# Kernel optimization log

Measured on AMD Instinct MI355X. Metric: run time of the kernel, lower is better.

Reference implementation:

```python
import jax, jax.numpy as jnp
import numpy as np

B, NQ, NC = 256, 15, 30          # pairs, query size, corpus size (= max_set_size)
EQ, EC = 45, 90                  # original directed edges per query / corpus graph
ENEW = NQ * (NC - NQ)            # edges added to pad each query graph
NPG = 2 * NC                     # nodes per pair after padding
N = B * NPG                      # 15360 total nodes
E = B * (EQ + EC + ENEW)         # 92160 total edges
D = 128                          # node_state_dim == filters_3
T = 64                           # transform_dim
N_PROP = 5
SK_ITERS, SK_TEMP = 10, 0.1


def _glorot(rng, shape):
    fan_in, fan_out = shape[0], shape[-1]
    s = np.sqrt(2.0 / (fan_in + fan_out))
    return jnp.asarray(rng.standard_normal(shape) * s, dtype=jnp.float32)


def setup_inputs() -> dict:
    rng = np.random.default_rng(0)
    frs, tos = [], []
    # original edges, grouped per pair as (query graph, corpus graph)
    for i in range(B):
        qoff, coff = i * NPG, i * NPG + NC
        frs.append(rng.integers(0, NQ, EQ) + qoff)
        tos.append(rng.integers(0, NQ, EQ) + qoff)
        frs.append(rng.integers(0, NC, EC) + coff)
        tos.append(rng.integers(0, NC, EC) + coff)
    # new padding edges: from each original query node to each new node
    for i in range(B):
        qoff = i * NPG
        frs.append(np.repeat(np.arange(NQ), NC - NQ) + qoff)
        tos.append(np.tile(np.arange(NQ, NC), NQ) + qoff)
    from_idx = jnp.asarray(np.concatenate(frs), dtype=jnp.int32)
    to_idx = jnp.asarray(np.concatenate(tos), dtype=jnp.int32)
    n_orig = B * (EQ + EC)
    mask_from_idx = jnp.concatenate([jnp.ones(n_orig), jnp.zeros(E - n_orig)]).astype(jnp.float32)
    inp = {
        'node_features': jnp.ones((N, 1), jnp.float32),
        'edge_features': jnp.ones((E, 1), jnp.float32),
        'mask_from_idx': mask_from_idx,
        'enc_node_w': _glorot(rng, (1, D)), 'enc_node_b': jnp.zeros(D, jnp.float32),
        'enc_edge_w': _glorot(rng, (1, D)), 'enc_edge_b': jnp.zeros(D, jnp.float32),
        'msg_w1': _glorot(rng, (3 * D, 2 * D)), 'msg_b1': jnp.zeros(2 * D, jnp.float32),
        'msg_w2': _glorot(rng, (2 * D, D)), 'msg_b2': jnp.zeros(D, jnp.float32),
        'upd_w1': _glorot(rng, (2 * D, 2 * D)), 'upd_b1': jnp.zeros(2 * D, jnp.float32),
        'upd_w2': _glorot(rng, (2 * D, D)), 'upd_b2': jnp.zeros(D, jnp.float32),
        'ft1_w': _glorot(rng, (D, T)), 'ft1_b': jnp.zeros(T, jnp.float32),
        'ft2_w': _glorot(rng, (T, T)), 'ft2_b': jnp.zeros(T, jnp.float32),
        'from_idx': from_idx, 'to_idx': to_idx,
    }
    return inp


def reference(node_features, edge_features, mask_from_idx,
              enc_node_w, enc_node_b, enc_edge_w, enc_edge_b,
              msg_w1, msg_b1, msg_w2, msg_b2,
              upd_w1, upd_b1, upd_w2, upd_b2,
              ft1_w, ft1_b, ft2_w, ft2_b,
              from_idx, to_idx):
    # GraphEncoder: linear embed of all-ones node/edge features
    h = node_features @ enc_node_w + enc_node_b          # [N, D]
    e = edge_features @ enc_edge_w + enc_edge_b          # [E, D]
    m = mask_from_idx[:, None]
    # shared GraphPropLayer applied n_prop_layers times
    for _ in range(N_PROP):
        msg_in = jnp.concatenate([h[from_idx], h[to_idx], e], axis=-1)      # [E, 3D]
        msg = jax.nn.relu(msg_in @ msg_w1 + msg_b1) @ msg_w2 + msg_b2       # [E, D]
        agg = jax.ops.segment_sum(msg * m, to_idx, num_segments=N)          # [N, D]
        upd_in = jnp.concatenate([agg, h], axis=-1)                          # [N, 2D]
        h = h + (jax.nn.relu(upd_in @ upd_w1 + upd_b1) @ upd_w2 + upd_b2)   # residual update
    hp = h.reshape(B, 2, NC, D)
    q_emb, c_emb = hp[:, 0], hp[:, 1]                    # [B, NC, D] each
    def transform(x):
        return jax.nn.relu(x @ ft1_w + ft1_b) @ ft2_w + ft2_b
    # query mask: only first NQ (original) nodes kept; corpus graphs are full size
    q_mask = (jnp.arange(NC) < NQ).astype(h.dtype)[None, :, None]
    tq = transform(q_emb) * q_mask                       # [B, NC, T]
    tc = transform(c_emb)                                # [B, NC, T]
    log_alpha = jnp.einsum('bqt,bct->bqc', tq, tc) / SK_TEMP
    for _ in range(SK_ITERS):
        log_alpha = log_alpha - jax.nn.logsumexp(log_alpha, axis=2, keepdims=True)
        log_alpha = log_alpha - jax.nn.logsumexp(log_alpha, axis=1, keepdims=True)
    tp = jnp.exp(log_alpha)                              # [B, NC, NC] transport plan
    moved = jnp.einsum('bqc,bcd->bqd', tp, c_emb)
    scores = -jnp.sum(jax.nn.relu(q_emb - moved), axis=(1, 2))  # [B]
    return scores
```

## Files before the change

kernel.cpp:

```cpp
#include <hip/hip_runtime.h>

#define BATCH 256
#define D 128
#define TT 64
#define NPG 60
#define NCC 30
#define NQQ 15
#define EPG 135
#define NPROP 5
#define SKI 10

typedef __attribute__((ext_vector_type(8))) short bf16x8;
typedef __attribute__((ext_vector_type(4))) float f32x4;

union U8 { bf16x8 v; uint4 u; };

__device__ __forceinline__ unsigned short f2bf(float f) {
    union { float f; unsigned int i; } t;
    t.f = f;
    unsigned int r = t.i + 0x7fffu + ((t.i >> 16) & 1u);
    return (unsigned short)(r >> 16);
}
__device__ __forceinline__ float bf2f(unsigned short u) {
    union { float f; unsigned int i; } t;
    t.i = ((unsigned int)u) << 16;
    return t.f;
}
__device__ __forceinline__ void split_bf(float v, unsigned short& hi, unsigned short& lo) {
    hi = f2bf(v);
    lo = f2bf(v - bf2f(hi));
}

__device__ __forceinline__ void splitv(float4 a, float4 b, bf16x8& hi, bf16x8& lo) {
    unsigned int ia0=__float_as_uint(a.x), ia1=__float_as_uint(a.y);
    unsigned int ia2=__float_as_uint(a.z), ia3=__float_as_uint(a.w);
    unsigned int ib0=__float_as_uint(b.x), ib1=__float_as_uint(b.y);
    unsigned int ib2=__float_as_uint(b.z), ib3=__float_as_uint(b.w);
    U8 uh, ul;
    uh.u = make_uint4((ia0>>16)|(ia1&0xffff0000u), (ia2>>16)|(ia3&0xffff0000u),
                      (ib0>>16)|(ib1&0xffff0000u), (ib2>>16)|(ib3&0xffff0000u));
    float r0 = a.x - __uint_as_float(ia0&0xffff0000u);
    float r1 = a.y - __uint_as_float(ia1&0xffff0000u);
    float r2 = a.z - __uint_as_float(ia2&0xffff0000u);
    float r3 = a.w - __uint_as_float(ia3&0xffff0000u);
    float r4 = b.x - __uint_as_float(ib0&0xffff0000u);
    float r5 = b.y - __uint_as_float(ib1&0xffff0000u);
    float r6 = b.z - __uint_as_float(ib2&0xffff0000u);
    float r7 = b.w - __uint_as_float(ib3&0xffff0000u);
    ul.u = make_uint4((__float_as_uint(r0)>>16)|(__float_as_uint(r1)&0xffff0000u),
                      (__float_as_uint(r2)>>16)|(__float_as_uint(r3)&0xffff0000u),
                      (__float_as_uint(r4)>>16)|(__float_as_uint(r5)&0xffff0000u),
                      (__float_as_uint(r6)>>16)|(__float_as_uint(r7)&0xffff0000u));
    hi = uh.v; lo = ul.v;
}

#define MFMA3(ah, al, bh, bl, acc)                                              \
    acc = __builtin_amdgcn_mfma_f32_16x16x32_bf16(ah, bh, acc, 0, 0, 0);        \
    acc = __builtin_amdgcn_mfma_f32_16x16x32_bf16(al, bh, acc, 0, 0, 0);        \
    acc = __builtin_amdgcn_mfma_f32_16x16x32_bf16(ah, bl, acc, 0, 0, 0);

__global__ void k_prep_uv(const float* __restrict__ ew, const float* __restrict__ eb,
                          const float* __restrict__ w1, const float* __restrict__ b1,
                          float* __restrict__ uv) {
    int t = threadIdx.x;
    float u = 0.f, v = 0.f;
    for (int d = 0; d < D; ++d) {
        float wv = w1[(256 + d) * 256 + t];
        u += ew[d] * wv;
        v += eb[d] * wv;
    }
    uv[t] = u;
    uv[256 + t] = v + b1[t];
}

__global__ void k_prep_w2(const float* __restrict__ mw1, const float* __restrict__ mw2,
                          const float* __restrict__ uw1, const float* __restrict__ uw2,
                          const float* __restrict__ f1w, const float* __restrict__ f2w,
                          unsigned short* __restrict__ w1h, unsigned short* __restrict__ w1l,
                          unsigned short* __restrict__ w2h, unsigned short* __restrict__ w2l,
                          unsigned short* __restrict__ u1h, unsigned short* __restrict__ u1l,
                          unsigned short* __restrict__ u2h, unsigned short* __restrict__ u2l,
                          unsigned short* __restrict__ g1h, unsigned short* __restrict__ g1l,
                          unsigned short* __restrict__ g2h, unsigned short* __restrict__ g2l) {
    int idx = blockIdx.x * 512 + threadIdx.x;
    int o, KS;
    unsigned short *ph, *pl;
    int mtype;
    if (idx < 65536)        { o = idx;          KS = 4; ph = w1h; pl = w1l; mtype = 0; }
    else if (idx < 98304)   { o = idx - 65536;  KS = 8; ph = w2h; pl = w2l; mtype = 1; }
    else if (idx < 163840)  { o = idx - 98304;  KS = 8; ph = u1h; pl = u1l; mtype = 2; }
    else if (idx < 196608)  { o = idx - 163840; KS = 8; ph = u2h; pl = u2l; mtype = 3; }
    else if (idx < 204800)  { o = idx - 196608; KS = 4; ph = g1h; pl = g1l; mtype = 4; }
    else if (idx < 208896)  { o = idx - 204800; KS = 2; ph = g2h; pl = g2l; mtype = 5; }
    else return;
    int t = o & 7;
    int l = (o >> 3) & 63;
    int frag = o >> 9;
    int ks = frag % KS;
    int nfr = frag / KS;
    int n = nfr * 16 + (l & 15);
    int k = ks * 32 + (l >> 4) * 8 + t;
    float v;
    switch (mtype) {
        case 0: v = (n < 256) ? mw1[k * 256 + n] : mw1[(128 + k) * 256 + (n - 256)]; break;
        case 1: v = mw2[k * 128 + n]; break;
        case 2: v = uw1[k * 256 + n]; break;
        case 3: v = uw2[k * 128 + n]; break;
        case 4: v = f1w[k * 64 + n]; break;
        default: v = f2w[k * 64 + n]; break;
    }
    unsigned short hi, lo;
    split_bf(v, hi, lo);
    ph[o] = hi;
    pl[o] = lo;
}

__global__ __launch_bounds__(512, 2) void k_mega(
    const float* __restrict__ nfeat, const float* __restrict__ efeat,
    const float* __restrict__ mfi,
    const float* __restrict__ enw, const float* __restrict__ enb,
    const float* __restrict__ uvg,
    const unsigned short* __restrict__ w1h, const unsigned short* __restrict__ w1l,
    const unsigned short* __restrict__ w2h, const unsigned short* __restrict__ w2l,
    const unsigned short* __restrict__ u1h, const unsigned short* __restrict__ u1l,
    const unsigned short* __restrict__ u2h, const unsigned short* __restrict__ u2l,
    const unsigned short* __restrict__ g1h, const unsigned short* __restrict__ g1l,
    const unsigned short* __restrict__ g2h, const unsigned short* __restrict__ g2l,
    const float* __restrict__ mb2, const float* __restrict__ ub1,
    const float* __restrict__ ub2, const float* __restrict__ f1b,
    const float* __restrict__ f2b,
    const int* __restrict__ fr, const int* __restrict__ to,
    float* __restrict__ out) {
    __shared__ __align__(16) float hS[60][132];
    __shared__ __align__(16) float H1S[45][516];
    __shared__ __align__(16) float aggS[45][132];
    __shared__ float uS[256], vS[256];
    __shared__ int cfS[144], ctS[144];
    __shared__ float efS[144], msS[144];
    __shared__ float b2S[128], ub1S[256], ub2S[128], f1bS[64], f2bS[64];

    int g = blockIdx.x;
    int tid = threadIdx.x;
    int wid = tid >> 6, lane = tid & 63;
    int l15 = lane & 15, l4 = lane >> 4;
    int rloc = l4 * 4;

    if (tid < 256) uS[tid] = uvg[tid];
    else vS[tid - 256] = uvg[tid];
    if (tid < 128) b2S[tid] = mb2[tid];
    if (tid < 256) ub1S[tid] = ub1[tid];
    if (tid < 128) ub2S[tid] = ub2[tid];
    if (tid < 64) { f1bS[tid] = f1b[tid]; f2bS[tid] = f2b[tid]; }
    if (tid < EPG) {
        int fn = fr[g * EPG + tid] - g * NPG;
        int tn = to[g * EPG + tid] - g * NPG;
        cfS[tid] = fn < 15 ? fn : fn - 15;
        ctS[tid] = tn < 15 ? tn : tn - 15;
        efS[tid] = efeat[g * EPG + tid];
        msS[tid] = mfi[g * EPG + tid];
    } else if (tid < 144) {
        cfS[tid] = 0; ctS[tid] = 0; efS[tid] = 0.f; msS[tid] = 0.f;
    }
    for (int i = tid; i < 60 * 128; i += 512) {
        int r = i >> 7, d = i & 127;
        hS[r][d] = nfeat[g * NPG + r] * enw[d] + enb[d];
    }
    __syncthreads();

    float* US = &H1S[0][0];
    char* zb = (char*)&aggS[0][0];

    for (int iter = 0; iter < NPROP; ++iter) {
        {
            f32x4 acc[3][4] = {};
#pragma unroll
            for (int ks = 0; ks < 4; ++ks) {
                int k0 = ks * 32 + l4 * 8;
                bf16x8 ah[3], al[3];
#pragma unroll
                for (int i = 0; i < 3; ++i) {
                    int r = i * 16 + l15;
                    int hr = r < 15 ? r : (r < 45 ? r + 15 : 0);
                    float4 a0 = *(const float4*)&hS[hr][k0];
                    float4 a1 = *(const float4*)&hS[hr][k0 + 4];
                    splitv(a0, a1, ah[i], al[i]);
                }
#pragma unroll
                for (int j = 0; j < 4; ++j) {
                    int nfr = wid * 4 + j;
                    int off = ((nfr * 4 + ks) * 64 + lane) * 8;
                    U8 th, tl;
                    th.u = *(const uint4*)(w1h + off);
                    tl.u = *(const uint4*)(w1l + off);
#pragma unroll
                    for (int i = 0; i < 3; ++i) { MFMA3(ah[i], al[i], th.v, tl.v, acc[i][j]); }
                }
            }
#pragma unroll
            for (int i = 0; i < 3; ++i)
#pragma unroll
                for (int j = 0; j < 4; ++j) {
                    int col = wid * 64 + j * 16 + l15;
#pragma unroll
                    for (int r = 0; r < 4; ++r) {
                        int m = i * 16 + rloc + r;
                        if (m < 45) H1S[m][col] = acc[i][j][r];
                    }
                }
        }
        __syncthreads();

        {
            bf16x8 WH[8], WL[8];
#pragma unroll
            for (int ks = 0; ks < 8; ++ks) {
                int off = ((wid * 8 + ks) * 64 + lane) * 8;
                U8 th, tl;
                th.u = *(const uint4*)(w2h + off);
                tl.u = *(const uint4*)(w2l + off);
                WH[ks] = th.v; WL[ks] = tl.v;
            }
            f32x4 accB[9] = {};
#pragma unroll
            for (int ks = 0; ks < 8; ++ks) {
                __syncthreads();
                for (int u = tid; u < 576; u += 512) {
                    int f = u >> 6, l = u & 63;
                    int e = f * 16 + (l & 15);
                    int k0 = ks * 32 + (l >> 4) * 8;
                    int ee = e < EPG ? e : 0;
                    int cf = cfS[ee], ct = ctS[ee];
                    float ev = e < EPG ? efS[ee] : 0.f;
                    float4 x0 = *(const float4*)&H1S[cf][k0];
                    float4 x1 = *(const float4*)&H1S[cf][k0 + 4];
                    float4 y0 = *(const float4*)&H1S[ct][256 + k0];
                    float4 y1 = *(const float4*)&H1S[ct][256 + k0 + 4];
                    x0.x = fmaxf(x0.x + y0.x + ev * uS[k0 + 0] + vS[k0 + 0], 0.f);
                    x0.y = fmaxf(x0.y + y0.y + ev * uS[k0 + 1] + vS[k0 + 1], 0.f);
                    x0.z = fmaxf(x0.z + y0.z + ev * uS[k0 + 2] + vS[k0 + 2], 0.f);
                    x0.w = fmaxf(x0.w + y0.w + ev * uS[k0 + 3] + vS[k0 + 3], 0.f);
                    x1.x = fmaxf(x1.x + y1.x + ev * uS[k0 + 4] + vS[k0 + 4], 0.f);
                    x1.y = fmaxf(x1.y + y1.y + ev * uS[k0 + 5] + vS[k0 + 5], 0.f);
                    x1.z = fmaxf(x1.z + y1.z + ev * uS[k0 + 6] + vS[k0 + 6], 0.f);
                    x1.w = fmaxf(x1.w + y1.w + ev * uS[k0 + 7] + vS[k0 + 7], 0.f);
                    bf16x8 zh, zl;
                    splitv(x0, x1, zh, zl);
                    U8 sh, sl; sh.v = zh; sl.v = zl;
                    *(uint4*)(zb + f * 2048 + l * 16) = sh.u;
                    *(uint4*)(zb + f * 2048 + 1024 + l * 16) = sl.u;
                }
                __syncthreads();
#pragma unroll
                for (int f = 0; f < 9; ++f) {
                    bf16x8 zh = *(bf16x8*)(zb + f * 2048 + lane * 16);
                    bf16x8 zl = *(bf16x8*)(zb + f * 2048 + 1024 + lane * 16);
                    MFMA3(zh, zl, WH[ks], WL[ks], accB[f]);
                }
            }
            __syncthreads();
            for (int i = tid; i < 45 * 132; i += 512) (&aggS[0][0])[i] = 0.f;
            __syncthreads();
            {
                int col = wid * 16 + l15;
                float bias = b2S[col];
#pragma unroll
                for (int f = 0; f < 9; ++f)
#pragma unroll
                    for (int r = 0; r < 4; ++r) {
                        int e = f * 16 + rloc + r;
                        if (e < EPG)
                            atomicAdd(&aggS[ctS[e]][col], (accB[f][r] + bias) * msS[e]);
                    }
            }
        }
        __syncthreads();

        {
            bf16x8 CH[2][8], CL[2][8];
#pragma unroll
            for (int j = 0; j < 2; ++j)
#pragma unroll
                for (int ks = 0; ks < 8; ++ks) {
                    int nfr = wid * 2 + j;
                    int off = ((nfr * 8 + ks) * 64 + lane) * 8;
                    U8 th, tl;
                    th.u = *(const uint4*)(u1h + off);
                    tl.u = *(const uint4*)(u1l + off);
                    CH[j][ks] = th.v; CL[j][ks] = tl.v;
                }
            f32x4 accC[4][2] = {};
#pragma unroll
            for (int ks = 0; ks < 8; ++ks) {
                int k0 = ks * 32 + l4 * 8;
#pragma unroll
                for (int mf = 0; mf < 4; ++mf) {
                    int p = mf * 16 + l15;
                    float4 z0, z1;
                    if (ks < 4) {
                        int ar = p < 15 ? p : (p < 60 ? p - 15 : 0);
                        z0 = *(const float4*)&aggS[ar][k0];
                        z1 = *(const float4*)&aggS[ar][k0 + 4];
                        float msk = (p >= 15 && p < 30) ? 0.f : 1.f;
                        z0.x *= msk; z0.y *= msk; z0.z *= msk; z0.w *= msk;
                        z1.x *= msk; z1.y *= msk; z1.z *= msk; z1.w *= msk;
                    } else {
                        int hr = p < 60 ? p : 0;
                        z0 = *(const float4*)&hS[hr][k0 - 128];
                        z1 = *(const float4*)&hS[hr][k0 - 128 + 4];
                    }
                    bf16x8 ah, al;
                    splitv(z0, z1, ah, al);
#pragma unroll
                    for (int j = 0; j < 2; ++j) { MFMA3(ah, al, CH[j][ks], CL[j][ks], accC[mf][j]); }
                }
            }
            __syncthreads();
#pragma unroll
            for (int mf = 0; mf < 4; ++mf)
#pragma unroll
                for (int j = 0; j < 2; ++j) {
                    int col = (wid * 2 + j) * 16 + l15;
                    float bias = ub1S[col];
#pragma unroll
                    for (int r = 0; r < 4; ++r) {
                        int m = mf * 16 + rloc + r;
                        if (m < 60) US[m * 260 + col] = fmaxf(accC[mf][j][r] + bias, 0.f);
                    }
                }
        }
        __syncthreads();

        {
            bf16x8 DH[8], DL[8];
#pragma unroll
            for (int ks = 0; ks < 8; ++ks) {
                int off = ((wid * 8 + ks) * 64 + lane) * 8;
                U8 th, tl;
                th.u = *(const uint4*)(u2h + off);
                tl.u = *(const uint4*)(u2l + off);
                DH[ks] = th.v; DL[ks] = tl.v;
            }
            f32x4 accD[4] = {};
#pragma unroll
            for (int ks = 0; ks < 8; ++ks) {
                int k0 = ks * 32 + l4 * 8;
#pragma unroll
                for (int mf = 0; mf < 4; ++mf) {
                    int p = mf * 16 + l15;
                    int pr = p < 60 ? p : 0;
                    float4 z0 = *(const float4*)&US[pr * 260 + k0];
                    float4 z1 = *(const float4*)&US[pr * 260 + k0 + 4];
                    bf16x8 ah, al;
                    splitv(z0, z1, ah, al);
                    MFMA3(ah, al, DH[ks], DL[ks], accD[mf]);
                }
            }
#pragma unroll
            for (int mf = 0; mf < 4; ++mf) {
                int col = wid * 16 + l15;
                float bias = ub2S[col];
#pragma unroll
                for (int r = 0; r < 4; ++r) {
                    int m = mf * 16 + rloc + r;
                    if (m < 60) hS[m][col] += accD[mf][r] + bias;
                }
            }
        }
        __syncthreads();
    }

    float* hid = &H1S[0][0];
    float* tS = hid + 45 * 68;
    float* la = &aggS[0][0];
    float* red = la + 1024;

    if (wid < 6) {
        int mf = wid >> 1, nh = wid & 1;
        f32x4 acc[2] = {};
#pragma unroll
        for (int ks = 0; ks < 4; ++ks) {
            int k0 = ks * 32 + l4 * 8;
            int r = mf * 16 + l15;
            int hr = r < 15 ? r : (r < 45 ? r + 15 : 0);
            float4 a0 = *(const float4*)&hS[hr][k0];
            float4 a1 = *(const float4*)&hS[hr][k0 + 4];
            bf16x8 ah, al;
            splitv(a0, a1, ah, al);
#pragma unroll
            for (int j = 0; j < 2; ++j) {
                int nfr = nh * 2 + j;
                int off = ((nfr * 4 + ks) * 64 + lane) * 8;
                U8 th, tl;
                th.u = *(const uint4*)(g1h + off);
                tl.u = *(const uint4*)(g1l + off);
                MFMA3(ah, al, th.v, tl.v, acc[j]);
            }
        }
#pragma unroll
        for (int j = 0; j < 2; ++j) {
            int col = nh * 32 + j * 16 + l15;
            float bias = f1bS[col];
#pragma unroll
            for (int r = 0; r < 4; ++r) {
                int m = mf * 16 + rloc + r;
                if (m < 45) hid[m * 68 + col] = fmaxf(acc[j][r] + bias, 0.f);
            }
        }
    }
    __syncthreads();
    if (wid < 6) {
        int mf = wid >> 1, nh = wid & 1;
        f32x4 acc[2] = {};
#pragma unroll
        for (int ks = 0; ks < 2; ++ks) {
            int k0 = ks * 32 + l4 * 8;
            int r = mf * 16 + l15;
            int hr = r < 45 ? r : 0;
            float4 a0 = *(const float4*)&hid[hr * 68 + k0];
            float4 a1 = *(const float4*)&hid[hr * 68 + k0 + 4];
            bf16x8 ah, al;
            splitv(a0, a1, ah, al);
#pragma unroll
            for (int j = 0; j < 2; ++j) {
                int nfr = nh * 2 + j;
                int off = ((nfr * 2 + ks) * 64 + lane) * 8;
                U8 th, tl;
                th.u = *(const uint4*)(g2h + off);
                tl.u = *(const uint4*)(g2l + off);
                MFMA3(ah, al, th.v, tl.v, acc[j]);
            }
        }
#pragma unroll
        for (int j = 0; j < 2; ++j) {
            int col = nh * 32 + j * 16 + l15;
            float bias = f2bS[col];
#pragma unroll
            for (int r = 0; r < 4; ++r) {
                int m = mf * 16 + rloc + r;
                if (m < 45) tS[m * 68 + col] = acc[j][r] + bias;
            }
        }
    }
    __syncthreads();
    for (int e = tid; e < NCC * NCC; e += 512) {
        int q = e / NCC, c = e % NCC;
        float s = 0.f;
        if (q < NQQ) {
#pragma unroll 4
            for (int k = 0; k < TT; k++) s += tS[q * 68 + k] * tS[(15 + c) * 68 + k];
            s *= 10.0f;
        }
        la[q * 33 + c] = s;
    }
    __syncthreads();
    int grp = tid >> 3, k8 = tid & 7;
    for (int it = 0; it < SKI; ++it) {
        if (grp < NCC) {
            float v0, v1, v2, v3, m;
            int c0 = k8 * 4;
            v0 = (c0 + 0 < NCC) ? la[grp * 33 + c0 + 0] : -INFINITY;
            v1 = (c0 + 1 < NCC) ? la[grp * 33 + c0 + 1] : -INFINITY;
            v2 = (c0 + 2 < NCC) ? la[grp * 33 + c0 + 2] : -INFINITY;
            v3 = (c0 + 3 < NCC) ? la[grp * 33 + c0 + 3] : -INFINITY;
            m = fmaxf(fmaxf(v0, v1), fmaxf(v2, v3));
            m = fmaxf(m, __shfl_xor(m, 1));
            m = fmaxf(m, __shfl_xor(m, 2));
            m = fmaxf(m, __shfl_xor(m, 4));
            float s = 0.f;
            if (c0 + 0 < NCC) s += __expf(v0 - m);
            if (c0 + 1 < NCC) s += __expf(v1 - m);
            if (c0 + 2 < NCC) s += __expf(v2 - m);
            if (c0 + 3 < NCC) s += __expf(v3 - m);
            s += __shfl_xor(s, 1);
            s += __shfl_xor(s, 2);
            s += __shfl_xor(s, 4);
            float lse = m + __logf(s);
            if (c0 + 0 < NCC) la[grp * 33 + c0 + 0] = v0 - lse;
            if (c0 + 1 < NCC) la[grp * 33 + c0 + 1] = v1 - lse;
            if (c0 + 2 < NCC) la[grp * 33 + c0 + 2] = v2 - lse;
            if (c0 + 3 < NCC) la[grp * 33 + c0 + 3] = v3 - lse;
        }
        __syncthreads();
        if (grp < NCC) {
            float v0, v1, v2, v3, m;
            int q0 = k8 * 4;
            v0 = (q0 + 0 < NCC) ? la[(q0 + 0) * 33 + grp] : -INFINITY;
            v1 = (q0 + 1 < NCC) ? la[(q0 + 1) * 33 + grp] : -INFINITY;
            v2 = (q0 + 2 < NCC) ? la[(q0 + 2) * 33 + grp] : -INFINITY;
            v3 = (q0 + 3 < NCC) ? la[(q0 + 3) * 33 + grp] : -INFINITY;
            m = fmaxf(fmaxf(v0, v1), fmaxf(v2, v3));
            m = fmaxf(m, __shfl_xor(m, 1));
            m = fmaxf(m, __shfl_xor(m, 2));
            m = fmaxf(m, __shfl_xor(m, 4));
            float s = 0.f;
            if (q0 + 0 < NCC) s += __expf(v0 - m);
            if (q0 + 1 < NCC) s += __expf(v1 - m);
            if (q0 + 2 < NCC) s += __expf(v2 - m);
            if (q0 + 3 < NCC) s += __expf(v3 - m);
            s += __shfl_xor(s, 1);
            s += __shfl_xor(s, 2);
            s += __shfl_xor(s, 4);
            float lse = m + __logf(s);
            if (q0 + 0 < NCC) la[(q0 + 0) * 33 + grp] = v0 - lse;
            if (q0 + 1 < NCC) la[(q0 + 1) * 33 + grp] = v1 - lse;
            if (q0 + 2 < NCC) la[(q0 + 2) * 33 + grp] = v2 - lse;
            if (q0 + 3 < NCC) la[(q0 + 3) * 33 + grp] = v3 - lse;
        }
        __syncthreads();
    }
    for (int e = tid; e < NCC * NCC; e += 512) {
        int q = e / NCC, c = e % NCC;
        la[q * 33 + c] = __expf(la[q * 33 + c]);
    }
    __syncthreads();
    float part = 0.f;
    for (int idx = tid; idx < NCC * D; idx += 512) {
        int q = idx >> 7, d = idx & 127;
        float mv = 0.f;
#pragma unroll 5
        for (int c = 0; c < NCC; c++) mv += la[q * 33 + c] * hS[30 + c][d];
        part += fmaxf(hS[q][d] - mv, 0.f);
    }
    red[tid] = part;
    __syncthreads();
    for (int s2 = 256; s2 > 0; s2 >>= 1) {
        if (tid < s2) red[tid] += red[tid + s2];
        __syncthreads();
    }
    if (tid == 0) out[g] = -red[0];
}

extern "C" void kernel_launch(void* const* d_in, const int* in_sizes, int n_in,
                              void* d_out, int out_size, void* d_ws, size_t ws_size,
                              hipStream_t stream) {
    const float* nf  = (const float*)d_in[0];
    const float* ef  = (const float*)d_in[1];
    const float* mfi = (const float*)d_in[2];
    const float* enw = (const float*)d_in[3];
    const float* enb = (const float*)d_in[4];
    const float* eew = (const float*)d_in[5];
    const float* eeb = (const float*)d_in[6];
    const float* mw1 = (const float*)d_in[7];
    const float* mb1 = (const float*)d_in[8];
    const float* mw2 = (const float*)d_in[9];
    const float* mb2 = (const float*)d_in[10];
    const float* uw1 = (const float*)d_in[11];
    const float* ub1 = (const float*)d_in[12];
    const float* uw2 = (const float*)d_in[13];
    const float* ub2 = (const float*)d_in[14];
    const float* f1w = (const float*)d_in[15];
    const float* f1b = (const float*)d_in[16];
    const float* f2w = (const float*)d_in[17];
    const float* f2b = (const float*)d_in[18];
    const int* fr = (const int*)d_in[19];
    const int* to = (const int*)d_in[20];
    float* out = (float*)d_out;

    char* base = (char*)d_ws;
    float* uv = (float*)base;
    unsigned short* w = (unsigned short*)(base + 4096);
    unsigned short* w1h = w;            unsigned short* w1l = w1h + 65536;
    unsigned short* w2h = w1l + 65536;  unsigned short* w2l = w2h + 32768;
    unsigned short* u1h = w2l + 32768;  unsigned short* u1l = u1h + 65536;
    unsigned short* u2h = u1l + 65536;  unsigned short* u2l = u2h + 32768;
    unsigned short* g1h = u2l + 32768;  unsigned short* g1l = g1h + 8192;
    unsigned short* g2h = g1l + 8192;   unsigned short* g2l = g2h + 4096;

    k_prep_uv<<<1, 256, 0, stream>>>(eew, eeb, mw1, mb1, uv);
    k_prep_w2<<<408, 512, 0, stream>>>(mw1, mw2, uw1, uw2, f1w, f2w,
                                       w1h, w1l, w2h, w2l, u1h, u1l, u2h, u2l,
                                       g1h, g1l, g2h, g2l);
    k_mega<<<BATCH, 512, 0, stream>>>(nf, ef, mfi, enw, enb, uv,
                                      w1h, w1l, w2h, w2l, u1h, u1l, u2h, u2l,
                                      g1h, g1l, g2h, g2l,
                                      mb2, ub1, ub2, f1b, f2b, fr, to, out);
}
```

Measured before the change: 370.7 us.

## Double block size to 1024 threads and re-split GEMM work across 16 waves

Launches the fused per-pair kernel with 1024 threads instead of 512 and redistributes the MFMA work in every stage (message MLP, edge GEMM, update MLP, feature transform) across 16 wavefronts, giving each wave fewer output fragments. The aim is more parallelism and latency hiding inside each block, since there are only 256 blocks on a GPU with many CUs. In exchange, each wave does less work per barrier, the edge GEMM is split unevenly (5 and 4 fragments), and register limits under launch_bounds(1024) may force spills or lower occupancy.

New measurement: 532.3 us. +43.6%, slower.

```diff
diff --git a/kernel.cpp b/kernel.cpp
--- a/kernel.cpp
+++ b/kernel.cpp
@@ -115,7 +115,7 @@
     pl[o] = lo;
 }
 
-__global__ __launch_bounds__(512, 2) void k_mega(
+__global__ __launch_bounds__(1024, 4) void k_mega(
     const float* __restrict__ nfeat, const float* __restrict__ efeat,
     const float* __restrict__ mfi,
     const float* __restrict__ enw, const float* __restrict__ enb,
@@ -146,7 +146,7 @@
     int rloc = l4 * 4;
 
     if (tid < 256) uS[tid] = uvg[tid];
-    else vS[tid - 256] = uvg[tid];
+    else if (tid < 512) vS[tid - 256] = uvg[tid];
     if (tid < 128) b2S[tid] = mb2[tid];
     if (tid < 256) ub1S[tid] = ub1[tid];
     if (tid < 128) ub2S[tid] = ub2[tid];
@@ -161,7 +161,7 @@
     } else if (tid < 144) {
         cfS[tid] = 0; ctS[tid] = 0; efS[tid] = 0.f; msS[tid] = 0.f;
     }
-    for (int i = tid; i < 60 * 128; i += 512) {
+    for (int i = tid; i < 60 * 128; i += 1024) {
         int r = i >> 7, d = i & 127;
         hS[r][d] = nfeat[g * NPG + r] * enw[d] + enb[d];
     }
@@ -172,7 +172,7 @@
 
     for (int iter = 0; iter < NPROP; ++iter) {
         {
-            f32x4 acc[3][4] = {};
+            f32x4 acc[3][2] = {};
 #pragma unroll
             for (int ks = 0; ks < 4; ++ks) {
                 int k0 = ks * 32 + l4 * 8;
@@ -186,8 +186,8 @@
                     splitv(a0, a1, ah[i], al[i]);
                 }
 #pragma unroll
-                for (int j = 0; j < 4; ++j) {
-                    int nfr = wid * 4 + j;
+                for (int j = 0; j < 2; ++j) {
+                    int nfr = wid * 2 + j;
                     int off = ((nfr * 4 + ks) * 64 + lane) * 8;
                     U8 th, tl;
                     th.u = *(const uint4*)(w1h + off);
@@ -199,8 +199,8 @@
 #pragma unroll
             for (int i = 0; i < 3; ++i)
 #pragma unroll
-                for (int j = 0; j < 4; ++j) {
-                    int col = wid * 64 + j * 16 + l15;
+                for (int j = 0; j < 2; ++j) {
+                    int col = (wid * 2 + j) * 16 + l15;
 #pragma unroll
                     for (int r = 0; r < 4; ++r) {
                         int m = i * 16 + rloc + r;
@@ -211,21 +211,24 @@
         __syncthreads();
 
         {
+            int mh = wid >> 3, nf = wid & 7;
+            int f0 = mh ? 5 : 0;
+            int fn = mh ? 4 : 5;
             bf16x8 WH[8], WL[8];
 #pragma unroll
             for (int ks = 0; ks < 8; ++ks) {
-                int off = ((wid * 8 + ks) * 64 + lane) * 8;
+                int off = ((nf * 8 + ks) * 64 + lane) * 8;
                 U8 th, tl;
                 th.u = *(const uint4*)(w2h + off);
                 tl.u = *(const uint4*)(w2l + off);
                 WH[ks] = th.v; WL[ks] = tl.v;
             }
-            f32x4 accB[9] = {};
+            f32x4 accB[5] = {};
 #pragma unroll
             for (int ks = 0; ks < 8; ++ks) {
                 __syncthreads();
-                for (int u = tid; u < 576; u += 512) {
-                    int f = u >> 6, l = u & 63;
+                if (tid < 576) {
+                    int f = tid >> 6, l = tid & 63;
                     int e = f * 16 + (l & 15);
                     int k0 = ks * 32 + (l >> 4) * 8;
                     int ee = e < EPG ? e : 0;
@@ -251,44 +254,47 @@
                 }
                 __syncthreads();
 #pragma unroll
-                for (int f = 0; f < 9; ++f) {
-                    bf16x8 zh = *(bf16x8*)(zb + f * 2048 + lane * 16);
-                    bf16x8 zl = *(bf16x8*)(zb + f * 2048 + 1024 + lane * 16);
-                    MFMA3(zh, zl, WH[ks], WL[ks], accB[f]);
+                for (int fi = 0; fi < 5; ++fi) {
+                    if (fi < fn) {
+                        int f = f0 + fi;
+                        bf16x8 zh = *(bf16x8*)(zb + f * 2048 + lane * 16);
+                        bf16x8 zl = *(bf16x8*)(zb + f * 2048 + 1024 + lane * 16);
+                        MFMA3(zh, zl, WH[ks], WL[ks], accB[fi]);
+                    }
                 }
             }
             __syncthreads();
-            for (int i = tid; i < 45 * 132; i += 512) (&aggS[0][0])[i] = 0.f;
+            for (int i = tid; i < 45 * 132; i += 1024) (&aggS[0][0])[i] = 0.f;
             __syncthreads();
             {
-                int col = wid * 16 + l15;
+                int col = nf * 16 + l15;
                 float bias = b2S[col];
 #pragma unroll
-                for (int f = 0; f < 9; ++f)
-#pragma unroll
-                    for (int r = 0; r < 4; ++r) {
-                        int e = f * 16 + rloc + r;
-                        if (e < EPG)
-                            atomicAdd(&aggS[ctS[e]][col], (accB[f][r] + bias) * msS[e]);
+                for (int fi = 0; fi < 5; ++fi) {
+                    if (fi < fn) {
+#pragma unroll
+                        for (int r = 0; r < 4; ++r) {
+                            int e = (f0 + fi) * 16 + rloc + r;
+                            if (e < EPG)
+                                atomicAdd(&aggS[ctS[e]][col], (accB[fi][r] + bias) * msS[e]);
+                        }
                     }
+                }
             }
         }
         __syncthreads();
 
         {
-            bf16x8 CH[2][8], CL[2][8];
-#pragma unroll
-            for (int j = 0; j < 2; ++j)
-#pragma unroll
-                for (int ks = 0; ks < 8; ++ks) {
-                    int nfr = wid * 2 + j;
-                    int off = ((nfr * 8 + ks) * 64 + lane) * 8;
-                    U8 th, tl;
-                    th.u = *(const uint4*)(u1h + off);
-                    tl.u = *(const uint4*)(u1l + off);
-                    CH[j][ks] = th.v; CL[j][ks] = tl.v;
-                }
-            f32x4 accC[4][2] = {};
+            bf16x8 CH[8], CL[8];
+#pragma unroll
+            for (int ks = 0; ks < 8; ++ks) {
+                int off = ((wid * 8 + ks) * 64 + lane) * 8;
+                U8 th, tl;
+                th.u = *(const uint4*)(u1h + off);
+                tl.u = *(const uint4*)(u1l + off);
+                CH[ks] = th.v; CL[ks] = tl.v;
+            }
+            f32x4 accC[4] = {};
 #pragma unroll
             for (int ks = 0; ks < 8; ++ks) {
                 int k0 = ks * 32 + l4 * 8;
@@ -310,59 +316,57 @@
                     }
                     bf16x8 ah, al;
                     splitv(z0, z1, ah, al);
-#pragma unroll
-                    for (int j = 0; j < 2; ++j) { MFMA3(ah, al, CH[j][ks], CL[j][ks], accC[mf][j]); }
+                    MFMA3(ah, al, CH[ks], CL[ks], accC[mf]);
                 }
             }
             __syncthreads();
 #pragma unroll
-            for (int mf = 0; mf < 4; ++mf)
-#pragma unroll
-                for (int j = 0; j < 2; ++j) {
-                    int col = (wid * 2 + j) * 16 + l15;
-                    float bias = ub1S[col];
-#pragma unroll
-                    for (int r = 0; r < 4; ++r) {
-                        int m = mf * 16 + rloc + r;
-                        if (m < 60) US[m * 260 + col] = fmaxf(accC[mf][j][r] + bias, 0.f);
-                    }
-                }
+            for (int mf = 0; mf < 4; ++mf) {
+                int col = wid * 16 + l15;
+                float bias = ub1S[col];
+#pragma unroll
+                for (int r = 0; r < 4; ++r) {
+                    int m = mf * 16 + rloc + r;
+                    if (m < 60) US[m * 260 + col] = fmaxf(accC[mf][r] + bias, 0.f);
+                }
+            }
         }
         __syncthreads();
 
         {
+            int mh = wid >> 3, nf = wid & 7;
             bf16x8 DH[8], DL[8];
 #pragma unroll
             for (int ks = 0; ks < 8; ++ks) {
-                int off = ((wid * 8 + ks) * 64 + lane) * 8;
+                int off = ((nf * 8 + ks) * 64 + lane) * 8;
                 U8 th, tl;
                 th.u = *(const uint4*)(u2h + off);
                 tl.u = *(const uint4*)(u2l + off);
                 DH[ks] = th.v; DL[ks] = tl.v;
             }
-            f32x4 accD[4] = {};
+            f32x4 accD[2] = {};
 #pragma unroll
             for (int ks = 0; ks < 8; ++ks) {
                 int k0 = ks * 32 + l4 * 8;
 #pragma unroll
-                for (int mf = 0; mf < 4; ++mf) {
-                    int p = mf * 16 + l15;
+                for (int mi = 0; mi < 2; ++mi) {
+                    int p = (mh * 2 + mi) * 16 + l15;
                     int pr = p < 60 ? p : 0;
                     float4 z0 = *(const float4*)&US[pr * 260 + k0];
                     float4 z1 = *(const float4*)&US[pr * 260 + k0 + 4];
                     bf16x8 ah, al;
                     splitv(z0, z1, ah, al);
-                    MFMA3(ah, al, DH[ks], DL[ks], accD[mf]);
-                }
-            }
-#pragma unroll
-            for (int mf = 0; mf < 4; ++mf) {
-                int col = wid * 16 + l15;
+                    MFMA3(ah, al, DH[ks], DL[ks], accD[mi]);
+                }
+            }
+#pragma unroll
+            for (int mi = 0; mi < 2; ++mi) {
+                int col = nf * 16 + l15;
                 float bias = ub2S[col];
 #pragma unroll
                 for (int r = 0; r < 4; ++r) {
-                    int m = mf * 16 + rloc + r;
-                    if (m < 60) hS[m][col] += accD[mf][r] + bias;
+                    int m = (mh * 2 + mi) * 16 + rloc + r;
+                    if (m < 60) hS[m][col] += accD[mi][r] + bias;
                 }
             }
         }
@@ -374,9 +378,9 @@
     float* la = &aggS[0][0];
     float* red = la + 1024;
 
-    if (wid < 6) {
-        int mf = wid >> 1, nh = wid & 1;
-        f32x4 acc[2] = {};
+    if (wid < 12) {
+        int mf = wid >> 2, nfr = wid & 3;
+        f32x4 acc = {};
 #pragma unroll
         for (int ks = 0; ks < 4; ++ks) {
             int k0 = ks * 32 + l4 * 8;
@@ -386,31 +390,24 @@
             float4 a1 = *(const float4*)&hS[hr][k0 + 4];
             bf16x8 ah, al;
             splitv(a0, a1, ah, al);
-#pragma unroll
-            for (int j = 0; j < 2; ++j) {
-                int nfr = nh * 2 + j;
-                int off = ((nfr * 4 + ks) * 64 + lane) * 8;
-                U8 th, tl;
-                th.u = *(const uint4*)(g1h + off);
-                tl.u = *(const uint4*)(g1l + off);
-                MFMA3(ah, al, th.v, tl.v, acc[j]);
-            }
-        }
-#pragma unroll
-        for (int j = 0; j < 2; ++j) {
-            int col = nh * 32 + j * 16 + l15;
-            float bias = f1bS[col];
-#pragma unroll
-            for (int r = 0; r < 4; ++r) {
-                int m = mf * 16 + rloc + r;
-                if (m < 45) hid[m * 68 + col] = fmaxf(acc[j][r] + bias, 0.f);
-            }
+            int off = ((nfr * 4 + ks) * 64 + lane) * 8;
+            U8 th, tl;
+            th.u = *(const uint4*)(g1h + off);
+            tl.u = *(const uint4*)(g1l + off);
+            MFMA3(ah, al, th.v, tl.v, acc);
+        }
+        int col = nfr * 16 + l15;
+        float bias = f1bS[col];
+#pragma unroll
+        for (int r = 0; r < 4; ++r) {
+            int m = mf * 16 + rloc + r;
+            if (m < 45) hid[m * 68 + col] = fmaxf(acc[r] + bias, 0.f);
         }
     }
     __syncthreads();
-    if (wid < 6) {
-        int mf = wid >> 1, nh = wid & 1;
-        f32x4 acc[2] = {};
+    if (wid < 12) {
+        int mf = wid >> 2, nfr = wid & 3;
+        f32x4 acc = {};
 #pragma unroll
         for (int ks = 0; ks < 2; ++ks) {
             int k0 = ks * 32 + l4 * 8;
@@ -420,29 +417,22 @@
             float4 a1 = *(const float4*)&hid[hr * 68 + k0 + 4];
             bf16x8 ah, al;
             splitv(a0, a1, ah, al);
-#pragma unroll
-            for (int j = 0; j < 2; ++j) {
-                int nfr = nh * 2 + j;
-                int off = ((nfr * 2 + ks) * 64 + lane) * 8;
-                U8 th, tl;
-                th.u = *(const uint4*)(g2h + off);
-                tl.u = *(const uint4*)(g2l + off);
-                MFMA3(ah, al, th.v, tl.v, acc[j]);
-            }
-        }
-#pragma unroll
-        for (int j = 0; j < 2; ++j) {
-            int col = nh * 32 + j * 16 + l15;
-            float bias = f2bS[col];
-#pragma unroll
-            for (int r = 0; r < 4; ++r) {
-                int m = mf * 16 + rloc + r;
-                if (m < 45) tS[m * 68 + col] = acc[j][r] + bias;
-            }
+            int off = ((nfr * 2 + ks) * 64 + lane) * 8;
+            U8 th, tl;
+            th.u = *(const uint4*)(g2h + off);
+            tl.u = *(const uint4*)(g2l + off);
+            MFMA3(ah, al, th.v, tl.v, acc);
+        }
+        int col = nfr * 16 + l15;
+        float bias = f2bS[col];
+#pragma unroll
+        for (int r = 0; r < 4; ++r) {
+            int m = mf * 16 + rloc + r;
+            if (m < 45) tS[m * 68 + col] = acc[r] + bias;
         }
     }
     __syncthreads();
-    for (int e = tid; e < NCC * NCC; e += 512) {
+    for (int e = tid; e < NCC * NCC; e += 1024) {
         int q = e / NCC, c = e % NCC;
         float s = 0.f;
         if (q < NQQ) {
@@ -508,13 +498,13 @@
         }
         __syncthreads();
     }
-    for (int e = tid; e < NCC * NCC; e += 512) {
+    for (int e = tid; e < NCC * NCC; e += 1024) {
         int q = e / NCC, c = e % NCC;
         la[q * 33 + c] = __expf(la[q * 33 + c]);
     }
     __syncthreads();
     float part = 0.f;
-    for (int idx = tid; idx < NCC * D; idx += 512) {
+    for (int idx = tid; idx < NCC * D; idx += 1024) {
         int q = idx >> 7, d = idx & 127;
         float mv = 0.f;
 #pragma unroll 5
@@ -523,7 +513,7 @@
     }
     red[tid] = part;
     __syncthreads();
-    for (int s2 = 256; s2 > 0; s2 >>= 1) {
+    for (int s2 = 512; s2 > 0; s2 >>= 1) {
         if (tid < s2) red[tid] += red[tid + s2];
         __syncthreads();
     }
@@ -570,8 +560,8 @@
     k_prep_w2<<<408, 512, 0, stream>>>(mw1, mw2, uw1, uw2, f1w, f2w,
                                        w1h, w1l, w2h, w2l, u1h, u1l, u2h, u2l,
                                        g1h, g1l, g2h, g2l);
-    k_mega<<<BATCH, 512, 0, stream>>>(nf, ef, mfi, enw, enb, uv,
-                                      w1h, w1l, w2h, w2l, u1h, u1l, u2h, u2l,
-                                      g1h, g1l, g2h, g2l,
-                                      mb2, ub1, ub2, f1b, f2b, fr, to, out);
-}
+    k_mega<<<BATCH, 1024, 0, stream>>>(nf, ef, mfi, enw, enb, uv,
+                                       w1h, w1l, w2h, w2l, u1h, u1l, u2h, u2l,
+                                       g1h, g1l, g2h, g2l,
+                                       mb2, ub1, ub2, f1b, f2b, fr, to, out);
+}
```
